# Kernel tuning notes

Hardware: AMD Instinct MI355X
Metric: run time of the kernel (lower is better)

Reference implementation:

```python
import jax, jax.numpy as jnp
import numpy as np

H, BS, NB, R, K = 2048, 128, 44, 64, 8   # hidden, block_size, num_blocks, basis_rank, top_k
B, S = 4, 2048
I = NB * BS                               # intermediate size = 5632


def setup_inputs() -> dict:
    key = jax.random.key(0)
    ks = jax.random.split(key, 10)
    N = B * S
    return {
        "hidden_states": jax.random.normal(ks[0], (B, S, H), jnp.float32),
        "active_idx": jax.random.randint(ks[1], (N, K), 0, NB, jnp.int32),
        "active_score": jax.random.uniform(ks[2], (N, K), dtype=jnp.float32),
        "gate_w": jax.random.normal(ks[3], (I, H), jnp.float32) * 0.02,
        "up_w": jax.random.normal(ks[4], (I, H), jnp.float32) * 0.02,
        "down_w": jax.random.normal(ks[5], (H, I), jnp.float32) * 0.02,
        "enc_w": jax.random.normal(ks[6], (R, H), jnp.float32) * 0.02,
        "enc_b": jnp.zeros((R,), jnp.float32),
        "decoder": jax.random.normal(ks[7], (NB, R, BS), jnp.float32) * 0.02,
        "basis_bias": jnp.zeros((NB, BS), jnp.float32),
        "comp_bias": jnp.zeros((H,), jnp.float32),
        "scale": jnp.array(1.0, jnp.float32),
    }


def reference(hidden_states, active_idx, active_score, gate_w, up_w, down_w,
              enc_w, enc_b, decoder, basis_bias, comp_bias, scale):
    Bb, Ss, Hh = hidden_states.shape
    N = Bb * Ss
    x = hidden_states.reshape(N, Hh)                          # [N, H]

    # routing weights: softmax over selected block scores (all idx valid here),
    # scattered into a dense per-token per-block weight map (duplicates accumulate)
    w = jax.nn.softmax(active_score, axis=-1)                 # [N, K]
    block_w = jnp.zeros((N, NB), x.dtype).at[
        jnp.arange(N)[:, None], active_idx].add(w)            # [N, NB]

    # gated SiLU MLP intermediate over all blocks (dense equivalent of the
    # per-token block gather-compute)
    act = jax.nn.silu(x @ gate_w.T) * (x @ up_w.T)            # [N, I]

    # low-rank basis compensation: latent -> per-block block_size channels
    latent = jax.nn.silu(x @ enc_w.T + enc_b)                 # [N, R]
    comp = jnp.einsum('nr,brc->nbc', latent, decoder) + basis_bias  # [N, NB, BS]

    act_b = act.reshape(N, NB, BS) + scale * comp             # [N, NB, BS]
    weighted = (act_b * block_w[:, :, None]).reshape(N, I)    # mask+weight inactive blocks to 0

    out = weighted @ down_w.T + comp_bias                     # scatter back via down proj
    return out.reshape(Bb, Ss, Hh)
```

## Files before the change

### kernel.cpp

```cpp
#include <hip/hip_runtime.h>

#define H_  2048
#define BS_ 128
#define NB_ 44
#define R_  64
#define K_  8
#define N_  8192
#define I_  5632
#define MT  64
#define TILES 32
#define DOWN_GRID 512
#define MT2 128
#define TILES_GU 16
#define GRID_GU (8 * 6 * TILES_GU)

typedef __bf16 bf16x8 __attribute__((ext_vector_type(8)));
typedef float  f32x4  __attribute__((ext_vector_type(4)));

__device__ __forceinline__ unsigned short f2bf(float f) {
  unsigned int u = __float_as_uint(f);
  u = (u + 0x7FFFu + ((u >> 16) & 1u)) >> 16;
  return (unsigned short)u;
}
__device__ __forceinline__ float bf2f(unsigned short s) {
  return __uint_as_float(((unsigned int)s) << 16);
}
__device__ __forceinline__ bf16x8 ld8(const unsigned short* p) {
  uint4 v = *reinterpret_cast<const uint4*>(p);
  return __builtin_bit_cast(bf16x8, v);
}
__device__ __forceinline__ bf16x8 lds8(const char* p) {
  uint4 v = *reinterpret_cast<const uint4*>(p);
  return __builtin_bit_cast(bf16x8, v);
}
__device__ __forceinline__ void gl16(const void* g, void* l) {
  __builtin_amdgcn_global_load_lds(
      (const __attribute__((address_space(1))) char*)g,
      (__attribute__((address_space(3))) char*)l, 16, 0, 0);
}
#define WAIT_VM(n) do { asm volatile("s_waitcnt vmcnt(" #n ")" ::: "memory"); \
                        __builtin_amdgcn_sched_barrier(0); } while (0)
#define WAIT_LGKM0 do { asm volatile("s_waitcnt lgkmcnt(0)" ::: "memory"); \
                        __builtin_amdgcn_sched_barrier(0); } while (0)
#define SBAR __builtin_amdgcn_s_barrier()

__global__ void cvt_xgu(const float* __restrict__ x, const float* __restrict__ gw,
                        const float* __restrict__ uw, const float* __restrict__ ew,
                        const float* __restrict__ dw,
                        unsigned short* __restrict__ xb,
                        unsigned short* __restrict__ gwb,
                        unsigned short* __restrict__ uwb,
                        unsigned short* __restrict__ ewb,
                        unsigned short* __restrict__ dwb) {
  const int NX4 = N_ * H_ / 4;
  const int NG4 = I_ * H_ / 4;
  const int NE4 = R_ * H_ / 4;
  const int ND4 = H_ * I_ / 4;
  int total = NX4 + 2 * NG4 + NE4 + ND4;
  int stride = gridDim.x * blockDim.x;
  for (int i = blockIdx.x * blockDim.x + threadIdx.x; i < total; i += stride) {
    if (i < NX4 + 2 * NG4 + NE4) {
      const float4* s; ushort4* d; int j;
      if (i < NX4)                  { s = (const float4*)x;  d = (ushort4*)xb;  j = i; }
      else if (i < NX4 + NG4)       { s = (const float4*)gw; d = (ushort4*)gwb; j = i - NX4; }
      else if (i < NX4 + 2 * NG4)   { s = (const float4*)uw; d = (ushort4*)uwb; j = i - NX4 - NG4; }
      else                          { s = (const float4*)ew; d = (ushort4*)ewb; j = i - NX4 - 2 * NG4; }
      float4 v = s[j];
      ushort4 o; o.x = f2bf(v.x); o.y = f2bf(v.y); o.z = f2bf(v.z); o.w = f2bf(v.w);
      d[j] = o;
    } else {
      int j = i - (NX4 + 2 * NG4 + NE4);
      float4 v = ((const float4*)dw)[j];
      int flat = j * 4;
      int h = flat / I_;
      int rem = flat - h * I_;
      int b = rem >> 7, k = rem & 127;
      ushort4 o; o.x = f2bf(v.x); o.y = f2bf(v.y); o.z = f2bf(v.z); o.w = f2bf(v.w);
      *(ushort4*)(dwb + ((size_t)b * H_ + h) * BS_ + k) = o;
    }
  }
}

__global__ void cvt_dec(const float* __restrict__ dec, unsigned short* __restrict__ decb) {
  int i = blockIdx.x * 256 + threadIdx.x;
  if (i >= NB_ * BS_ * R_) return;
  int b = i >> 13;
  int rem = i & 8191;
  int c = rem >> 6, r = rem & 63;
  decb[i] = f2bf(dec[(b << 13) + r * BS_ + c]);
}

__global__ void zero_counts(int* __restrict__ counts) {
  if (threadIdx.x < NB_) counts[threadIdx.x] = 0;
}

__global__ void prep_kernel(const float* __restrict__ score,
                            const int* __restrict__ aidx,
                            float* __restrict__ w_buf,
                            int* __restrict__ counts) {
  __shared__ int hist[NB_];
  int tid = threadIdx.x;
  if (tid < NB_) hist[tid] = 0;
  __syncthreads();
  int n = blockIdx.x * 256 + tid;
  float s[K_];
  float m = -1e30f;
#pragma unroll
  for (int k = 0; k < K_; k++) { s[k] = score[n * K_ + k]; m = fmaxf(m, s[k]); }
  float sum = 0.f;
#pragma unroll
  for (int k = 0; k < K_; k++) { s[k] = __expf(s[k] - m); sum += s[k]; }
  float inv = 1.f / sum;
#pragma unroll
  for (int k = 0; k < K_; k++) {
    w_buf[n * K_ + k] = s[k] * inv;
    atomicAdd(&hist[aidx[n * K_ + k]], 1);
  }
  __syncthreads();
  if (tid < NB_) atomicAdd(&counts[tid], hist[tid]);
}

__global__ void scan_kernel(const int* __restrict__ counts,
                            int* __restrict__ offsets,
                            int* __restrict__ cursors) {
  if (threadIdx.x == 0) {
    int acc = 0;
    for (int b = 0; b < NB_; b++) { offsets[b] = acc; cursors[b] = acc; acc += counts[b]; }
    offsets[NB_] = acc;
  }
}

__global__ void fill_kernel(const int* __restrict__ aidx,
                            const float* __restrict__ w_buf,
                            int* __restrict__ cursors,
                            int* __restrict__ tok_list,
                            float* __restrict__ wt_list,
                            int* __restrict__ inv) {
  int n = blockIdx.x * 256 + threadIdx.x;
#pragma unroll
  for (int k = 0; k < K_; k++) {
    int b = aidx[n * K_ + k];
    int pos = atomicAdd(&cursors[b], 1);
    tok_list[pos] = n;
    wt_list[pos] = w_buf[n * K_ + k];
    inv[n * K_ + k] = pos;
  }
}

__global__ __launch_bounds__(256) void latent_mfma(
    const unsigned short* __restrict__ xb,
    const unsigned short* __restrict__ ewb,
    float* __restrict__ lat_part) {
  __shared__ __align__(16) char smem[16384];
  int tid = threadIdx.x;
  int wv = tid >> 6, lane = tid & 63;
  int lo = lane & 15, hi = lane >> 4;
  int grp = blockIdx.x >> 2, ksl = blockIdx.x & 3;
  int n0 = grp * 64;
  int k0 = ksl * 512;

  int rowA = tid >> 2;
  int jA = (tid & 3) ^ ((rowA >> 1) & 3);
  const unsigned short* srcA = xb + (size_t)(n0 + rowA) * H_ + k0 + jA * 8;
  const unsigned short* srcB = ewb + (size_t)rowA * H_ + k0 + jA * 8;

  gl16(srcA, smem + wv * 1024);
  gl16(srcB, smem + 8192 + wv * 1024);

  f32x4 acc[4] = {};
  int cur = 0;
  for (int ks = 0; ks < 512; ks += 32) {
    if (ks + 32 < 512) {
      gl16(srcA + ks + 32, smem + (cur ^ 1) * 4096 + wv * 1024);
      gl16(srcB + ks + 32, smem + 8192 + (cur ^ 1) * 4096 + wv * 1024);
      WAIT_VM(2);
    } else {
      WAIT_VM(0);
    }
    SBAR;
    int rB = wv * 16 + lo;
    bf16x8 Bf = lds8(smem + 8192 + cur * 4096 + (rB * 4 + (hi ^ ((rB >> 1) & 3))) * 16);
#pragma unroll
    for (int m = 0; m < 4; m++) {
      int row = m * 16 + lo;
      bf16x8 Af = lds8(smem + cur * 4096 + (row * 4 + (hi ^ ((row >> 1) & 3))) * 16);
      acc[m] = __builtin_amdgcn_mfma_f32_16x16x32_bf16(Af, Bf, acc[m], 0, 0, 0);
    }
    WAIT_LGKM0;
    SBAR;
    cur ^= 1;
  }

  int r = wv * 16 + lo;
  float* dst = lat_part + (size_t)ksl * N_ * R_;
#pragma unroll
  for (int m = 0; m < 4; m++) {
#pragma unroll
    for (int rg = 0; rg < 4; rg++) {
      int tok = n0 + m * 16 + hi * 4 + rg;
      dst[(size_t)tok * R_ + r] = acc[m][rg];
    }
  }
}

__global__ void latent_combine(const float* __restrict__ lp,
                               const float* __restrict__ enc_b,
                               unsigned short* __restrict__ lat) {
  const int T = N_ * R_;
  int i = blockIdx.x * 256 + threadIdx.x;
  if (i >= T) return;
  float v = lp[i] + lp[T + i] + lp[2 * T + i] + lp[3 * T + i] + enc_b[i & (R_ - 1)];
  lat[i] = f2bf(v / (1.f + __expf(-v)));
}

__device__ __forceinline__ bool decode_bt(int p, int& b, int& tile) {
  b = (p & 7) + 8 * ((p >> 3) / TILES);
  tile = (p >> 3) % TILES;
  return b < NB_;
}
__device__ __forceinline__ bool decode_bt_gu(int p, int& b, int& tile) {
  b = (p & 7) + 8 * ((p >> 3) / TILES_GU);
  tile = (p >> 3) % TILES_GU;
  return b < NB_;
}

__global__ __launch_bounds__(512, 4) void gateup_kernel(
    const unsigned short* __restrict__ xb,
    const unsigned short* __restrict__ gwb,
    const unsigned short* __restrict__ uwb,
    const unsigned short* __restrict__ latb,
    const unsigned short* __restrict__ decb_all,
    const float* __restrict__ bbias,
    const float* __restrict__ scale_p,
    const int* __restrict__ counts,
    const int* __restrict__ offsets,
    const int* __restrict__ tok_list,
    const float* __restrict__ wt_list,
    unsigned short* __restrict__ actw) {
  int b, tile;
  if (!decode_bt_gu(blockIdx.x, b, tile)) return;
  int cnt = counts[b];
  int base = tile * MT2;
  if (base >= cnt) return;
  int off = offsets[b];

  __shared__ __align__(16) char smem[49152];

  int tid = threadIdx.x;
  int wv = tid >> 6, lane = tid & 63;
  int lo = lane & 15, hi = lane >> 4;
  int wr = wv >> 2, wc = wv & 3;

  int rowA = tid >> 2;
  int jA = (tid & 3) ^ ((rowA >> 1) & 3);
  int tokA = tok_list[off + min(base + rowA, cnt - 1)];
  const unsigned short* srcA = xb + (size_t)tokA * H_ + jA * 8;

  const unsigned short* gb = gwb + (size_t)b * BS_ * H_;
  const unsigned short* ub = uwb + (size_t)b * BS_ * H_;
  int cS = tid >> 2;
  int jS = (tid & 3) ^ ((cS >> 1) & 3);
  const unsigned short* srcG = gb + (size_t)cS * H_ + jS * 8;
  const unsigned short* srcU = ub + (size_t)cS * H_ + jS * 8;

  f32x4 accG[4][2] = {};
  f32x4 accU[4][2] = {};

  gl16(srcA, smem + wv * 1024);
  gl16(srcG, smem + 16384 + wv * 1024);
  gl16(srcU, smem + 32768 + wv * 1024);

  for (int it = 0; it < 64; ++it) {
    int ks = it * 32;
    if (it < 63) {
      int nb_ = (it + 1) & 1;
      gl16(srcA + ks + 32, smem + nb_ * 8192 + wv * 1024);
      gl16(srcG + ks + 32, smem + 16384 + nb_ * 8192 + wv * 1024);
      gl16(srcU + ks + 32, smem + 32768 + nb_ * 8192 + wv * 1024);
      WAIT_VM(3);
    } else {
      WAIT_VM(0);
    }
    SBAR;
    int cur = it & 1;
    bf16x8 Af[4];
#pragma unroll
    for (int m = 0; m < 4; m++) {
      int row = wr * 64 + m * 16 + lo;
      int off16 = row * 4 + (hi ^ ((row >> 1) & 3));
      Af[m] = lds8(smem + cur * 8192 + off16 * 16);
    }
    bf16x8 Gf[2], Uf[2];
#pragma unroll
    for (int cf = 0; cf < 2; cf++) {
      int c = wc * 32 + cf * 16 + lo;
      int off16 = c * 4 + (hi ^ ((c >> 1) & 3));
      Gf[cf] = lds8(smem + 16384 + cur * 8192 + off16 * 16);
      Uf[cf] = lds8(smem + 32768 + cur * 8192 + off16 * 16);
    }
#pragma unroll
    for (int m = 0; m < 4; m++) {
#pragma unroll
      for (int cf = 0; cf < 2; cf++) {
        accG[m][cf] = __builtin_amdgcn_mfma_f32_16x16x32_bf16(Af[m], Gf[cf], accG[m][cf], 0, 0, 0);
        accU[m][cf] = __builtin_amdgcn_mfma_f32_16x16x32_bf16(Af[m], Uf[cf], accU[m][cf], 0, 0, 0);
      }
    }
    WAIT_LGKM0;
    SBAR;
  }

#pragma unroll
  for (int s = 0; s < 2; s++) {
    int o = s * 512 + tid;
    int r_ = o >> 3;
    int j = (o & 7) ^ (r_ & 7);
    int tokL = tok_list[off + min(base + r_, cnt - 1)];
    gl16(latb + (size_t)tokL * R_ + j * 8, smem + 32768 + s * 8192 + wv * 1024);
  }
  const unsigned short* decb = decb_all + (size_t)b * BS_ * R_;
#pragma unroll
  for (int s = 0; s < 2; s++) {
    int o = s * 512 + tid;
    int c = o >> 3;
    int j = (o & 7) ^ (c & 7);
    gl16(decb + (size_t)c * R_ + j * 8, smem + 16384 + s * 8192 + wv * 1024);
  }
  __syncthreads();

  f32x4 accC[4][2] = {};
#pragma unroll
  for (int kk = 0; kk < 2; kk++) {
    bf16x8 L[4];
#pragma unroll
    for (int m = 0; m < 4; m++) {
      int row = wr * 64 + m * 16 + lo;
      int off16 = row * 8 + ((kk * 4 + hi) ^ (row & 7));
      L[m] = lds8(smem + 32768 + off16 * 16);
    }
#pragma unroll
    for (int cf = 0; cf < 2; cf++) {
      int c = wc * 32 + cf * 16 + lo;
      int off16 = c * 8 + ((kk * 4 + hi) ^ (c & 7));
      bf16x8 D = lds8(smem + 16384 + off16 * 16);
#pragma unroll
      for (int m = 0; m < 4; m++)
        accC[m][cf] = __builtin_amdgcn_mfma_f32_16x16x32_bf16(L[m], D, accC[m][cf], 0, 0, 0);
    }
  }

  float scal = scale_p[0];
  int cc[2] = { wc * 32 + lo, wc * 32 + 16 + lo };
  float bbv[2] = { bbias[b * BS_ + cc[0]], bbias[b * BS_ + cc[1]] };
#pragma unroll
  for (int m = 0; m < 4; m++) {
#pragma unroll
    for (int r = 0; r < 4; r++) {
      int t = wr * 64 + m * 16 + hi * 4 + r;
      int g = base + t;
      if (g < cnt) {
        float wt = wt_list[off + g];
        unsigned short* dst = actw + (size_t)(off + g) * BS_;
#pragma unroll
        for (int cf = 0; cf < 2; cf++) {
          float gg = accG[m][cf][r];
          float uu = accU[m][cf][r];
          float act = (gg / (1.f + __expf(-gg))) * uu;
          dst[cc[cf]] = f2bf((act + scal * (accC[m][cf][r] + bbv[cf])) * wt);
        }
      }
    }
  }
}

__global__ __launch_bounds__(256) void down_kernel(
    const unsigned short* __restrict__ actw,
    const unsigned short* __restrict__ dwb,
    const int* __restrict__ counts,
    const int* __restrict__ offsets,
    unsigned short* __restrict__ partial,
    int hc0, int Hc) {
  __shared__ __align__(16) unsigned short a_lds[MT * BS_];
  __shared__ __align__(16) char b_lds[2][16384];
  int tid = threadIdx.x;
  int wv = tid >> 6, lane = tid & 63;
  int lo = lane & 15, hi = lane >> 4;
  int rs = tid >> 4;
  int jc = tid & 15;

  for (int p = blockIdx.x; p < 8 * 6 * TILES; p += DOWN_GRID) {
    int b, tile;
    if (!decode_bt(p, b, tile)) continue;
    int cnt = counts[b];
    int base = tile * MT;
    if (base >= cnt) continue;
    int off = offsets[b];

    for (int i = tid; i < MT * BS_ / 8; i += 256) {
      int t = i >> 4, cb = i & 15;
      int g = base + t;
      uint4 v = make_uint4(0, 0, 0, 0);
      if (g < cnt) v = *(const uint4*)(actw + (size_t)(off + g) * BS_ + cb * 8);
      *(uint4*)(&a_lds[t * BS_ + ((cb ^ (t & 7)) << 3)]) = v;
    }
    __syncthreads();

    bf16x8 Bf[4][4];
#pragma unroll
    for (int kst = 0; kst < 4; kst++)
#pragma unroll
      for (int sf = 0; sf < 4; sf++) {
        int t = sf * 16 + lo, cb = kst * 4 + hi;
        Bf[kst][sf] = ld8(&a_lds[t * BS_ + ((cb ^ (t & 7)) << 3)]);
      }

    const unsigned short* db = dwb + (size_t)b * H_ * BS_;
    {
      const unsigned short* d0 = db + (size_t)hc0 * BS_;
#pragma unroll
      for (int s = 0; s < 4; s++) {
        int r = s * 16 + rs;
        int j = jc ^ (r & 15);
        gl16(d0 + (size_t)r * BS_ + j * 8, b_lds[0] + s * 4096 + wv * 1024);
      }
    }
    __syncthreads();

    int nit = Hc >> 6;
    int cur = 0;
    for (int it = 0; it < nit; it++) {
      if (it + 1 < nit) {
        const unsigned short* dn = db + (size_t)(hc0 + (it + 1) * 64) * BS_;
#pragma unroll
        for (int s = 0; s < 4; s++) {
          int r = s * 16 + rs;
          int j = jc ^ (r & 15);
          gl16(dn + (size_t)r * BS_ + j * 8, b_lds[cur ^ 1] + s * 4096 + wv * 1024);
        }
      }
      f32x4 acc[4] = {};
      int rl = wv * 16 + lo;
#pragma unroll
      for (int kst = 0; kst < 4; kst++) {
        int cb = kst * 4 + hi;
        bf16x8 Aw = lds8(b_lds[cur] + (rl * 16 + (cb ^ lo)) * 16);
#pragma unroll
        for (int sf = 0; sf < 4; sf++)
          acc[sf] = __builtin_amdgcn_mfma_f32_16x16x32_bf16(Aw, Bf[kst][sf], acc[sf], 0, 0, 0);
      }
      int hrel = it * 64 + wv * 16 + hi * 4;
#pragma unroll
      for (int sf = 0; sf < 4; sf++) {
        int g = base + sf * 16 + lo;
        if (g < cnt) {
          uint2 pk;
          pk.x = (unsigned int)f2bf(acc[sf][0]) | ((unsigned int)f2bf(acc[sf][1]) << 16);
          pk.y = (unsigned int)f2bf(acc[sf][2]) | ((unsigned int)f2bf(acc[sf][3]) << 16);
          *(uint2*)(partial + (size_t)(off + g) * Hc + hrel) = pk;
        }
      }
      __syncthreads();
      cur ^= 1;
    }
  }
}

__global__ __launch_bounds__(256) void reduce_kernel(
    const unsigned short* __restrict__ partial,
    const int* __restrict__ inv,
    const float* __restrict__ cbias,
    float* __restrict__ out, int hc0, int Hc) {
  int wv = threadIdx.x >> 6, l = threadIdx.x & 63;
  int n = blockIdx.x * 4 + wv;
  int rows[K_];
#pragma unroll
  for (int k = 0; k < K_; k++) rows[k] = inv[n * K_ + k];
  for (int c0w = 0; c0w < Hc; c0w += 512) {
    int cw = c0w + l * 8;
    if (cw >= Hc) continue;
    float a[8] = {0.f, 0.f, 0.f, 0.f, 0.f, 0.f, 0.f, 0.f};
#pragma unroll
    for (int k = 0; k < K_; k++) {
      uint4 v = *(const uint4*)(partial + (size_t)rows[k] * Hc + cw);
      unsigned int w0 = v.x, w1 = v.y, w2 = v.z, w3 = v.w;
      a[0] += __uint_as_float(w0 << 16); a[1] += __uint_as_float(w0 & 0xFFFF0000u);
      a[2] += __uint_as_float(w1 << 16); a[3] += __uint_as_float(w1 & 0xFFFF0000u);
      a[4] += __uint_as_float(w2 << 16); a[5] += __uint_as_float(w2 & 0xFFFF0000u);
      a[6] += __uint_as_float(w3 << 16); a[7] += __uint_as_float(w3 & 0xFFFF0000u);
    }
    int h = hc0 + cw;
    float4 c0 = *(const float4*)(cbias + h);
    float4 c1 = *(const float4*)(cbias + h + 4);
    float4 o0 = make_float4(a[0] + c0.x, a[1] + c0.y, a[2] + c0.z, a[3] + c0.w);
    float4 o1 = make_float4(a[4] + c1.x, a[5] + c1.y, a[6] + c1.z, a[7] + c1.w);
    *(float4*)(out + (size_t)n * H_ + h) = o0;
    *(float4*)(out + (size_t)n * H_ + h + 4) = o1;
  }
}

extern "C" void kernel_launch(void* const* d_in, const int* in_sizes, int n_in,
                              void* d_out, int out_size, void* d_ws, size_t ws_size,
                              hipStream_t stream) {
  const float* x       = (const float*)d_in[0];
  const int*   aidx    = (const int*)d_in[1];
  const float* score   = (const float*)d_in[2];
  const float* gate_w  = (const float*)d_in[3];
  const float* up_w    = (const float*)d_in[4];
  const float* down_w  = (const float*)d_in[5];
  const float* enc_w   = (const float*)d_in[6];
  const float* enc_b   = (const float*)d_in[7];
  const float* decoder = (const float*)d_in[8];
  const float* bbias   = (const float*)d_in[9];
  const float* cbias   = (const float*)d_in[10];
  const float* scale   = (const float*)d_in[11];
  float* out = (float*)d_out;

  char* ws = (char*)d_ws;
  const size_t OFF_GWB  = 33554432ull;
  const size_t OFF_UWB  = 56623104ull;
  const size_t OFF_DEC  = 79691776ull;
  const size_t OFF_LATB = 80412672ull;
  const size_t OFF_ENCB = 81461248ull;
  const size_t OFF_WBUF = 81723392ull;
  const size_t OFF_TOK  = 81985536ull;
  const size_t OFF_WT   = 82247680ull;
  const size_t OFF_INV  = 82509824ull;
  const size_t OFF_CNT  = 82771968ull;
  const size_t OFF_ACTW = 82772992ull;
  const size_t BASE_END = 99550208ull;
  const size_t DWB_SZ   = 23068672ull;
  const size_t PART_FULL = 268435456ull;

  unsigned short* xb   = (unsigned short*)(ws);
  unsigned short* gwb  = (unsigned short*)(ws + OFF_GWB);
  unsigned short* uwb  = (unsigned short*)(ws + OFF_UWB);
  unsigned short* decb = (unsigned short*)(ws + OFF_DEC);
  unsigned short* latb = (unsigned short*)(ws + OFF_LATB);
  unsigned short* ewb  = (unsigned short*)(ws + OFF_ENCB);
  float* w_buf         = (float*)(ws + OFF_WBUF);
  int*   tok_list      = (int*)(ws + OFF_TOK);
  float* wt_list       = (float*)(ws + OFF_WT);
  int*   inv           = (int*)(ws + OFF_INV);
  int*   counts        = (int*)(ws + OFF_CNT);
  int*   offsets       = counts + 64;
  int*   cursors       = counts + 128;
  unsigned short* actw = (unsigned short*)(ws + OFF_ACTW);

  unsigned short* dwb  = (unsigned short*)(ws + BASE_END);
  unsigned short* partial = (unsigned short*)(ws + BASE_END + DWB_SZ);
  float* lat_part      = (float*)(ws + BASE_END + DWB_SZ);

  bool full = ws_size >= BASE_END + DWB_SZ + PART_FULL;

  cvt_xgu<<<2048, 256, 0, stream>>>(x, gate_w, up_w, enc_w, down_w,
                                    xb, gwb, uwb, ewb, dwb);
  cvt_dec<<<(NB_ * BS_ * R_ + 255) / 256, 256, 0, stream>>>(decoder, decb);
  zero_counts<<<1, 64, 0, stream>>>(counts);
  prep_kernel<<<N_ / 256, 256, 0, stream>>>(score, aidx, w_buf, counts);
  scan_kernel<<<1, 64, 0, stream>>>(counts, offsets, cursors);
  fill_kernel<<<N_ / 256, 256, 0, stream>>>(aidx, w_buf, cursors, tok_list, wt_list, inv);
  latent_mfma<<<N_ / 16, 256, 0, stream>>>(xb, ewb, lat_part);
  latent_combine<<<N_ * R_ / 256, 256, 0, stream>>>(lat_part, enc_b, latb);
  gateup_kernel<<<GRID_GU, 512, 0, stream>>>(xb, gwb, uwb, latb, decb, bbias, scale,
                                             counts, offsets, tok_list, wt_list, actw);
  if (full) {
    down_kernel<<<DOWN_GRID, 256, 0, stream>>>(actw, dwb, counts, offsets, partial, 0, H_);
    reduce_kernel<<<N_ / 4, 256, 0, stream>>>(partial, inv, cbias, out, 0, H_);
  } else {
    for (int c = 0; c < 4; c++) {
      down_kernel<<<DOWN_GRID, 256, 0, stream>>>(actw, dwb, counts, offsets, partial, c * 512, 512);
      reduce_kernel<<<N_ / 4, 256, 0, stream>>>(partial, inv, cbias, out, c * 512, 512);
    }
  }
}
```

Measured before the change: 546.1 us.

## Fuse down projection and reduction into one cooperative kernel with grid syncs

Replaces the separate down_kernel and reduce_kernel launches with a single cooperative kernel. It loops over four hidden-dimension chunks, and a grid-wide sync separates each chunk's down-projection GEMM from its top-k reduction. Each chunk's partial results go to a separate slice of the full-size buffer, so the partials for a chunk may still be cache-resident when they are reduced. The cost is grid.sync barriers, and the kernel depends on all 512 blocks being co-resident; if the cooperative launch fails it falls back to the chunked multi-launch path.

Result: no change. 538.3 us (-1.4%).

```diff
diff --git a/kernel.cpp b/kernel.cpp
--- a/kernel.cpp
+++ b/kernel.cpp
@@ -1,4 +1,7 @@
 #include <hip/hip_runtime.h>
+#include <hip/hip_cooperative_groups.h>
+
+namespace cg = cooperative_groups;
 
 #define H_  2048
 #define BS_ 128
@@ -10,6 +13,7 @@
 #define MT  64
 #define TILES 32
 #define DOWN_GRID 512
+#define HC  512
 #define MT2 128
 #define TILES_GU 16
 #define GRID_GU (8 * 6 * TILES_GU)
@@ -21,9 +25,6 @@
   unsigned int u = __float_as_uint(f);
   u = (u + 0x7FFFu + ((u >> 16) & 1u)) >> 16;
   return (unsigned short)u;
-}
-__device__ __forceinline__ float bf2f(unsigned short s) {
-  return __uint_as_float(((unsigned int)s) << 16);
 }
 __device__ __forceinline__ bf16x8 ld8(const unsigned short* p) {
   uint4 v = *reinterpret_cast<const uint4*>(p);
@@ -373,13 +374,16 @@
   }
 }
 
-__global__ __launch_bounds__(256) void down_kernel(
+__global__ __launch_bounds__(256) void downred_kernel(
     const unsigned short* __restrict__ actw,
     const unsigned short* __restrict__ dwb,
     const int* __restrict__ counts,
     const int* __restrict__ offsets,
+    const int* __restrict__ inv,
+    const float* __restrict__ cbias,
     unsigned short* __restrict__ partial,
-    int hc0, int Hc) {
+    float* __restrict__ out) {
+  cg::grid_group grid = cg::this_grid();
   __shared__ __align__(16) unsigned short a_lds[MT * BS_];
   __shared__ __align__(16) char b_lds[2][16384];
   int tid = threadIdx.x;
@@ -388,6 +392,130 @@
   int rs = tid >> 4;
   int jc = tid & 15;
 
+  for (int c = 0; c < H_ / HC; c++) {
+    int hc0 = c * HC;
+    unsigned short* pchunk = partial + (size_t)c * 65536 * HC;
+
+    for (int p = blockIdx.x; p < 8 * 6 * TILES; p += DOWN_GRID) {
+      int b, tile;
+      if (!decode_bt(p, b, tile)) continue;
+      int cnt = counts[b];
+      int base = tile * MT;
+      if (base >= cnt) continue;
+      int off = offsets[b];
+
+      for (int i = tid; i < MT * BS_ / 8; i += 256) {
+        int t = i >> 4, cb = i & 15;
+        int g = base + t;
+        uint4 v = make_uint4(0, 0, 0, 0);
+        if (g < cnt) v = *(const uint4*)(actw + (size_t)(off + g) * BS_ + cb * 8);
+        *(uint4*)(&a_lds[t * BS_ + ((cb ^ (t & 7)) << 3)]) = v;
+      }
+      __syncthreads();
+
+      bf16x8 Bf[4][4];
+#pragma unroll
+      for (int kst = 0; kst < 4; kst++)
+#pragma unroll
+        for (int sf = 0; sf < 4; sf++) {
+          int t = sf * 16 + lo, cb = kst * 4 + hi;
+          Bf[kst][sf] = ld8(&a_lds[t * BS_ + ((cb ^ (t & 7)) << 3)]);
+        }
+
+      const unsigned short* db = dwb + (size_t)b * H_ * BS_;
+      {
+        const unsigned short* d0 = db + (size_t)hc0 * BS_;
+#pragma unroll
+        for (int s = 0; s < 4; s++) {
+          int r = s * 16 + rs;
+          int j = jc ^ (r & 15);
+          gl16(d0 + (size_t)r * BS_ + j * 8, b_lds[0] + s * 4096 + wv * 1024);
+        }
+      }
+      __syncthreads();
+
+      int cur = 0;
+      for (int it = 0; it < HC / 64; it++) {
+        if (it + 1 < HC / 64) {
+          const unsigned short* dn = db + (size_t)(hc0 + (it + 1) * 64) * BS_;
+#pragma unroll
+          for (int s = 0; s < 4; s++) {
+            int r = s * 16 + rs;
+            int j = jc ^ (r & 15);
+            gl16(dn + (size_t)r * BS_ + j * 8, b_lds[cur ^ 1] + s * 4096 + wv * 1024);
+          }
+        }
+        f32x4 acc[4] = {};
+        int rl = wv * 16 + lo;
+#pragma unroll
+        for (int kst = 0; kst < 4; kst++) {
+          int cb = kst * 4 + hi;
+          bf16x8 Aw = lds8(b_lds[cur] + (rl * 16 + (cb ^ lo)) * 16);
+#pragma unroll
+          for (int sf = 0; sf < 4; sf++)
+            acc[sf] = __builtin_amdgcn_mfma_f32_16x16x32_bf16(Aw, Bf[kst][sf], acc[sf], 0, 0, 0);
+        }
+        int hrel = it * 64 + wv * 16 + hi * 4;
+#pragma unroll
+        for (int sf = 0; sf < 4; sf++) {
+          int g = base + sf * 16 + lo;
+          if (g < cnt) {
+            uint2 pk;
+            pk.x = (unsigned int)f2bf(acc[sf][0]) | ((unsigned int)f2bf(acc[sf][1]) << 16);
+            pk.y = (unsigned int)f2bf(acc[sf][2]) | ((unsigned int)f2bf(acc[sf][3]) << 16);
+            *(uint2*)(pchunk + (size_t)(off + g) * HC + hrel) = pk;
+          }
+        }
+        __syncthreads();
+        cur ^= 1;
+      }
+    }
+
+    grid.sync();
+
+    for (int n = blockIdx.x * 4 + wv; n < N_; n += DOWN_GRID * 4) {
+      int rows[K_];
+#pragma unroll
+      for (int k = 0; k < K_; k++) rows[k] = inv[n * K_ + k];
+      int cw = lane * 8;
+      float a[8] = {0.f, 0.f, 0.f, 0.f, 0.f, 0.f, 0.f, 0.f};
+#pragma unroll
+      for (int k = 0; k < K_; k++) {
+        uint4 v = *(const uint4*)(pchunk + (size_t)rows[k] * HC + cw);
+        unsigned int w0 = v.x, w1 = v.y, w2 = v.z, w3 = v.w;
+        a[0] += __uint_as_float(w0 << 16); a[1] += __uint_as_float(w0 & 0xFFFF0000u);
+        a[2] += __uint_as_float(w1 << 16); a[3] += __uint_as_float(w1 & 0xFFFF0000u);
+        a[4] += __uint_as_float(w2 << 16); a[5] += __uint_as_float(w2 & 0xFFFF0000u);
+        a[6] += __uint_as_float(w3 << 16); a[7] += __uint_as_float(w3 & 0xFFFF0000u);
+      }
+      int h = hc0 + cw;
+      float4 c0 = *(const float4*)(cbias + h);
+      float4 c1 = *(const float4*)(cbias + h + 4);
+      float4 o0 = make_float4(a[0] + c0.x, a[1] + c0.y, a[2] + c0.z, a[3] + c0.w);
+      float4 o1 = make_float4(a[4] + c1.x, a[5] + c1.y, a[6] + c1.z, a[7] + c1.w);
+      *(float4*)(out + (size_t)n * H_ + h) = o0;
+      *(float4*)(out + (size_t)n * H_ + h + 4) = o1;
+    }
+
+    grid.sync();
+  }
+}
+
+__global__ __launch_bounds__(256) void down_kernel(
+    const unsigned short* __restrict__ actw,
+    const unsigned short* __restrict__ dwb,
+    const int* __restrict__ counts,
+    const int* __restrict__ offsets,
+    unsigned short* __restrict__ partial,
+    int hc0) {
+  __shared__ __align__(16) unsigned short a_lds[MT * BS_];
+  __shared__ __align__(16) char b_lds[2][16384];
+  int tid = threadIdx.x;
+  int wv = tid >> 6, lane = tid & 63;
+  int lo = lane & 15, hi = lane >> 4;
+  int rs = tid >> 4;
+  int jc = tid & 15;
+
   for (int p = blockIdx.x; p < 8 * 6 * TILES; p += DOWN_GRID) {
     int b, tile;
     if (!decode_bt(p, b, tile)) continue;
@@ -426,10 +554,9 @@
     }
     __syncthreads();
 
-    int nit = Hc >> 6;
     int cur = 0;
-    for (int it = 0; it < nit; it++) {
-      if (it + 1 < nit) {
+    for (int it = 0; it < HC / 64; it++) {
+      if (it + 1 < HC / 64) {
         const unsigned short* dn = db + (size_t)(hc0 + (it + 1) * 64) * BS_;
 #pragma unroll
         for (int s = 0; s < 4; s++) {
@@ -456,7 +583,7 @@
           uint2 pk;
           pk.x = (unsigned int)f2bf(acc[sf][0]) | ((unsigned int)f2bf(acc[sf][1]) << 16);
           pk.y = (unsigned int)f2bf(acc[sf][2]) | ((unsigned int)f2bf(acc[sf][3]) << 16);
-          *(uint2*)(partial + (size_t)(off + g) * Hc + hrel) = pk;
+          *(uint2*)(partial + (size_t)(off + g) * HC + hrel) = pk;
         }
       }
       __syncthreads();
@@ -469,33 +596,30 @@
     const unsigned short* __restrict__ partial,
     const int* __restrict__ inv,
     const float* __restrict__ cbias,
-    float* __restrict__ out, int hc0, int Hc) {
+    float* __restrict__ out, int hc0) {
   int wv = threadIdx.x >> 6, l = threadIdx.x & 63;
   int n = blockIdx.x * 4 + wv;
   int rows[K_];
 #pragma unroll
   for (int k = 0; k < K_; k++) rows[k] = inv[n * K_ + k];
-  for (int c0w = 0; c0w < Hc; c0w += 512) {
-    int cw = c0w + l * 8;
-    if (cw >= Hc) continue;
-    float a[8] = {0.f, 0.f, 0.f, 0.f, 0.f, 0.f, 0.f, 0.f};
-#pragma unroll
-    for (int k = 0; k < K_; k++) {
-      uint4 v = *(const uint4*)(partial + (size_t)rows[k] * Hc + cw);
-      unsigned int w0 = v.x, w1 = v.y, w2 = v.z, w3 = v.w;
-      a[0] += __uint_as_float(w0 << 16); a[1] += __uint_as_float(w0 & 0xFFFF0000u);
-      a[2] += __uint_as_float(w1 << 16); a[3] += __uint_as_float(w1 & 0xFFFF0000u);
-      a[4] += __uint_as_float(w2 << 16); a[5] += __uint_as_float(w2 & 0xFFFF0000u);
-      a[6] += __uint_as_float(w3 << 16); a[7] += __uint_as_float(w3 & 0xFFFF0000u);
-    }
-    int h = hc0 + cw;
-    float4 c0 = *(const float4*)(cbias + h);
-    float4 c1 = *(const float4*)(cbias + h + 4);
-    float4 o0 = make_float4(a[0] + c0.x, a[1] + c0.y, a[2] + c0.z, a[3] + c0.w);
-    float4 o1 = make_float4(a[4] + c1.x, a[5] + c1.y, a[6] + c1.z, a[7] + c1.w);
-    *(float4*)(out + (size_t)n * H_ + h) = o0;
-    *(float4*)(out + (size_t)n * H_ + h + 4) = o1;
-  }
+  int cw = l * 8;
+  float a[8] = {0.f, 0.f, 0.f, 0.f, 0.f, 0.f, 0.f, 0.f};
+#pragma unroll
+  for (int k = 0; k < K_; k++) {
+    uint4 v = *(const uint4*)(partial + (size_t)rows[k] * HC + cw);
+    unsigned int w0 = v.x, w1 = v.y, w2 = v.z, w3 = v.w;
+    a[0] += __uint_as_float(w0 << 16); a[1] += __uint_as_float(w0 & 0xFFFF0000u);
+    a[2] += __uint_as_float(w1 << 16); a[3] += __uint_as_float(w1 & 0xFFFF0000u);
+    a[4] += __uint_as_float(w2 << 16); a[5] += __uint_as_float(w2 & 0xFFFF0000u);
+    a[6] += __uint_as_float(w3 << 16); a[7] += __uint_as_float(w3 & 0xFFFF0000u);
+  }
+  int h = hc0 + cw;
+  float4 c0 = *(const float4*)(cbias + h);
+  float4 c1 = *(const float4*)(cbias + h + 4);
+  float4 o0 = make_float4(a[0] + c0.x, a[1] + c0.y, a[2] + c0.z, a[3] + c0.w);
+  float4 o1 = make_float4(a[4] + c1.x, a[5] + c1.y, a[6] + c1.z, a[7] + c1.w);
+  *(float4*)(out + (size_t)n * H_ + h) = o0;
+  *(float4*)(out + (size_t)n * H_ + h + 4) = o1;
 }
 
 extern "C" void kernel_launch(void* const* d_in, const int* in_sizes, int n_in,
@@ -546,9 +670,9 @@
   int*   cursors       = counts + 128;
   unsigned short* actw = (unsigned short*)(ws + OFF_ACTW);
 
-  unsigned short* dwb  = (unsigned short*)(ws + BASE_END);
+  unsigned short* dwb     = (unsigned short*)(ws + BASE_END);
   unsigned short* partial = (unsigned short*)(ws + BASE_END + DWB_SZ);
-  float* lat_part      = (float*)(ws + BASE_END + DWB_SZ);
+  float* lat_part         = (float*)(ws + BASE_END + DWB_SZ);
 
   bool full = ws_size >= BASE_END + DWB_SZ + PART_FULL;
 
@@ -563,13 +687,20 @@
   latent_combine<<<N_ * R_ / 256, 256, 0, stream>>>(lat_part, enc_b, latb);
   gateup_kernel<<<GRID_GU, 512, 0, stream>>>(xb, gwb, uwb, latb, decb, bbias, scale,
                                              counts, offsets, tok_list, wt_list, actw);
+
+  bool coop_done = false;
   if (full) {
-    down_kernel<<<DOWN_GRID, 256, 0, stream>>>(actw, dwb, counts, offsets, partial, 0, H_);
-    reduce_kernel<<<N_ / 4, 256, 0, stream>>>(partial, inv, cbias, out, 0, H_);
-  } else {
-    for (int c = 0; c < 4; c++) {
-      down_kernel<<<DOWN_GRID, 256, 0, stream>>>(actw, dwb, counts, offsets, partial, c * 512, 512);
-      reduce_kernel<<<N_ / 4, 256, 0, stream>>>(partial, inv, cbias, out, c * 512, 512);
-    }
-  }
-}
+    void* args[] = { (void*)&actw, (void*)&dwb, (void*)&counts, (void*)&offsets,
+                     (void*)&inv, (void*)&cbias, (void*)&partial, (void*)&out };
+    hipError_t rc = hipLaunchCooperativeKernel((const void*)downred_kernel,
+                                               dim3(DOWN_GRID), dim3(256),
+                                               args, 0, stream);
+    coop_done = (rc == hipSuccess);
+  }
+  if (!coop_done) {
+    for (int c = 0; c < H_ / HC; c++) {
+      down_kernel<<<DOWN_GRID, 256, 0, stream>>>(actw, dwb, counts, offsets, partial, c * HC);
+      reduce_kernel<<<N_ / 4, 256, 0, stream>>>(partial, inv, cbias, out, c * HC);
+    }
+  }
+}
```
